# Optimization experiments

Measured on AMD Instinct MI355X. Metric: run time of the kernel, lower is better.

The kernel has to match this reference:

```python
import jax, jax.numpy as jnp
import numpy as np

N_HEAD = 8
HIDDENS = 512
NEG_INF = -1e9


def setup_inputs() -> dict:
    key = jax.random.key(0)
    ks = jax.random.split(key, 10)
    B, L, KVP, QP, H, W = 8, 1024, 512, 512, 32, 32
    s = 0.02  # init scale
    return {
        "v": jax.random.normal(ks[0], (B, L, KVP), jnp.float32),
        "k": jax.random.normal(ks[1], (B, L, KVP), jnp.float32),
        "q": jax.random.normal(ks[2], (B, QP, H, W), jnp.float32),
        "mask": jax.random.randint(ks[3], (B, 1, 1, L), 0, 2) > 0,
        "Wv": jax.random.normal(ks[4], (HIDDENS, KVP), jnp.float32) * s,
        "bv": jnp.zeros((HIDDENS,), jnp.float32),
        "Wk": jax.random.normal(ks[5], (HIDDENS, KVP), jnp.float32) * s,
        "bk": jnp.zeros((HIDDENS,), jnp.float32),
        "Wq": jax.random.normal(ks[6], (HIDDENS, QP), jnp.float32) * s,
        "bq": jnp.zeros((HIDDENS,), jnp.float32),
        "Wm": jax.random.normal(ks[7], (512, HIDDENS), jnp.float32) * s,
        "bm": jnp.zeros((512,), jnp.float32),
    }


def reference(v, k, q, mask, Wv, bv, Wk, bk, Wq, bq, Wm, bm):
    B, _, H, W = q.shape
    nh, dh = N_HEAD, HIDDENS // N_HEAD
    # k/v linear projections -> [B, nh, L, dh]
    vh = (v @ Wv.T + bv).reshape(B, -1, nh, dh).transpose(0, 2, 1, 3)
    kh = (k @ Wk.T + bk).reshape(B, -1, nh, dh).transpose(0, 2, 1, 3)
    # q 1x1 conv projection -> [B, hiddens, H, W] -> [B, nh, HW, dh]
    qp = jnp.einsum('bchw,oc->bohw', q, Wq) + bq[None, :, None, None]
    qh = qp.reshape(B, nh, dh, H * W).transpose(0, 1, 3, 2)
    # attention: scores fully materialized [B, nh, HW, L]
    scores = jnp.einsum('bnqd,bnkd->bnqk', qh, kh) / jnp.sqrt(jnp.float32(dh))
    scores = jnp.where(mask, NEG_INF, scores)
    att = jax.nn.softmax(scores, axis=-1)  # dropout omitted (eval mode)
    out = jnp.einsum('bnqk,bnkd->bnqd', att, vh)
    # [B, nh, HW, dh] -> [B, hiddens, H, W]
    out = out.transpose(0, 1, 3, 2).reshape(B, HIDDENS, H, W)
    out = jnp.einsum('bchw,oc->bohw', out, Wm) + bm[None, :, None, None]
    return jax.nn.relu(out)
```

## Files before the change

kernel.cpp:

```cpp
#include <hip/hip_runtime.h>

typedef __attribute__((ext_vector_type(8))) __bf16 bf16x8;
typedef __attribute__((ext_vector_type(4))) float  f32x4;

__device__ __forceinline__ unsigned short f2bf(float f) {
    unsigned int u = __builtin_bit_cast(unsigned int, f);
    u += 0x7fffu + ((u >> 16) & 1u);
    return (unsigned short)(u >> 16);
}
__device__ __forceinline__ unsigned int pack2(float a, float b) {
    return (unsigned int)f2bf(a) | ((unsigned int)f2bf(b) << 16);
}

__device__ __forceinline__ int swz8(int row, int chunk) {
    return row * 64 + ((chunk ^ (row & 7)) << 3);
}

__device__ __forceinline__ bf16x8 fragld(const unsigned short* lds, int row, int kk, int lane) {
    return *(const bf16x8*)(lds + swz8(row, kk * 4 + (lane >> 4)));
}

__device__ __forceinline__ void stage_direct_f32(unsigned short* lds, const float* g,
                                                 int ldg, int tid) {
#pragma unroll
    for (int s = 0; s < 2; ++s) {
        int idx = tid + s * 256;
        int row = idx >> 3, c = idx & 7;
        const float* gp = g + (size_t)row * ldg + c * 8;
        float4 v0 = *(const float4*)gp;
        float4 v1 = *(const float4*)(gp + 4);
        uint4 wr4;
        wr4.x = pack2(v0.x, v0.y); wr4.y = pack2(v0.z, v0.w);
        wr4.z = pack2(v1.x, v1.y); wr4.w = pack2(v1.z, v1.w);
        *(uint4*)(lds + swz8(row, c)) = wr4;
    }
}
__device__ __forceinline__ void stage_direct_bf16(unsigned short* lds, const unsigned short* g,
                                                  int ldg, int tid) {
#pragma unroll
    for (int s = 0; s < 2; ++s) {
        int idx = tid + s * 256;
        int row = idx >> 3, c = idx & 7;
        uint4 v = *(const uint4*)(g + (size_t)row * ldg + c * 8);
        *(uint4*)(lds + swz8(row, c)) = v;
    }
}
__device__ __forceinline__ void stage_trans_f32(unsigned short* lds, const float* g,
                                                int ldg, int tid) {
    int tk = (tid >> 4) * 4;
    int tn = (tid & 15) * 4;
    float rr[4][4];
#pragma unroll
    for (int i = 0; i < 4; ++i) {
        float4 v = *(const float4*)(g + (size_t)(tk + i) * ldg + tn);
        rr[i][0] = v.x; rr[i][1] = v.y; rr[i][2] = v.z; rr[i][3] = v.w;
    }
#pragma unroll
    for (int j = 0; j < 4; ++j) {
        int row = tn + j;
        uint2 w2;
        w2.x = pack2(rr[0][j], rr[1][j]);
        w2.y = pack2(rr[2][j], rr[3][j]);
        int off = row * 64 + (((tk >> 3) ^ (row & 7)) << 3) + (tk & 7);
        *(uint2*)(lds + off) = w2;
    }
}
__device__ __forceinline__ void stage_trans_bf16(unsigned short* lds, const unsigned short* g,
                                                 int ldg, int tid) {
    int tk = (tid >> 4) * 4;
    int tn = (tid & 15) * 4;
    unsigned short rr[4][4];
#pragma unroll
    for (int i = 0; i < 4; ++i) {
        ushort4 v = *(const ushort4*)(g + (size_t)(tk + i) * ldg + tn);
        rr[i][0] = v.x; rr[i][1] = v.y; rr[i][2] = v.z; rr[i][3] = v.w;
    }
#pragma unroll
    for (int j = 0; j < 4; ++j) {
        int row = tn + j;
        ushort4 w4;
        w4.x = rr[0][j]; w4.y = rr[1][j]; w4.z = rr[2][j]; w4.w = rr[3][j];
        int off = row * 64 + (((tk >> 3) ^ (row & 7)) << 3) + (tk & 7);
        *(ushort4*)(lds + off) = w4;
    }
}

#define MFMA_STEP(As, Bs)                                                        \
    _Pragma("unroll")                                                            \
    for (int kk = 0; kk < 2; ++kk) {                                             \
        bf16x8 a0 = fragld(As, r0w + (lane & 15), kk, lane);                     \
        bf16x8 a1 = fragld(As, r0w + 16 + (lane & 15), kk, lane);                \
        bf16x8 b0 = fragld(Bs, c0w + (lane & 15), kk, lane);                     \
        bf16x8 b1 = fragld(Bs, c0w + 16 + (lane & 15), kk, lane);                \
        acc[0][0] = __builtin_amdgcn_mfma_f32_16x16x32_bf16(a0, b0, acc[0][0], 0, 0, 0); \
        acc[0][1] = __builtin_amdgcn_mfma_f32_16x16x32_bf16(a0, b1, acc[0][1], 0, 0, 0); \
        acc[1][0] = __builtin_amdgcn_mfma_f32_16x16x32_bf16(a1, b0, acc[1][0], 0, 0, 0); \
        acc[1][1] = __builtin_amdgcn_mfma_f32_16x16x32_bf16(a1, b1, acc[1][1], 0, 0, 0); \
    }

__global__ __launch_bounds__(256) void k_proj_kv(const float* __restrict__ X,
                                                 const float* __restrict__ W,
                                                 const float* __restrict__ bias,
                                                 unsigned short* __restrict__ out) {
    __shared__ alignas(16) unsigned short As[64 * 64];
    __shared__ alignas(16) unsigned short Bs[64 * 64];
    int tid = threadIdx.x, lane = tid & 63, wid = tid >> 6;
    int r0w = (wid >> 1) * 32, c0w = (wid & 1) * 32;
    int m0 = blockIdx.x * 64, n0 = blockIdx.y * 64;
    f32x4 acc[2][2] = {};
    for (int kt = 0; kt < 512; kt += 64) {
        stage_direct_f32(As, X + (size_t)m0 * 512 + kt, 512, tid);
        stage_direct_f32(Bs, W + (size_t)n0 * 512 + kt, 512, tid);
        __syncthreads();
        MFMA_STEP(As, Bs)
        __syncthreads();
    }
#pragma unroll
    for (int j = 0; j < 2; ++j) {
        int o = n0 + c0w + j * 16 + (lane & 15);
        float bb = bias[o];
        int n = o >> 6, d = o & 63;
#pragma unroll
        for (int i = 0; i < 2; ++i) {
#pragma unroll
            for (int reg = 0; reg < 4; ++reg) {
                int r = m0 + r0w + i * 16 + ((lane >> 4) << 2) + reg;
                int b = r >> 10, l = r & 1023;
                out[(((size_t)(b * 8 + n)) * 1024 + l) * 64 + d] = f2bf(acc[i][j][reg] + bb);
            }
        }
    }
}

__global__ __launch_bounds__(256) void k_proj_q(const float* __restrict__ Q,
                                                const float* __restrict__ Wq,
                                                const float* __restrict__ bq,
                                                unsigned short* __restrict__ qh) {
    __shared__ alignas(16) unsigned short As[64 * 64];
    __shared__ alignas(16) unsigned short Bs[64 * 64];
    int tid = threadIdx.x, lane = tid & 63, wid = tid >> 6;
    int r0w = (wid >> 1) * 32, c0w = (wid & 1) * 32;
    int b = blockIdx.z;
    int m0 = blockIdx.x * 64;
    int n0 = blockIdx.y * 64;
    const float* Qb = Q + (size_t)b * 512 * 1024;
    f32x4 acc[2][2] = {};
    for (int kt = 0; kt < 512; kt += 64) {
        stage_trans_f32(As, Qb + (size_t)kt * 1024 + m0, 1024, tid);
        stage_direct_f32(Bs, Wq + (size_t)n0 * 512 + kt, 512, tid);
        __syncthreads();
        MFMA_STEP(As, Bs)
        __syncthreads();
    }
#pragma unroll
    for (int j = 0; j < 2; ++j) {
        int o = n0 + c0w + j * 16 + (lane & 15);
        float bb = bq[o];
        int n = o >> 6, d = o & 63;
#pragma unroll
        for (int i = 0; i < 2; ++i) {
#pragma unroll
            for (int reg = 0; reg < 4; ++reg) {
                int p = m0 + r0w + i * 16 + ((lane >> 4) << 2) + reg;
                qh[(((size_t)(b * 8 + n)) * 1024 + p) * 64 + d] =
                    f2bf((acc[i][j][reg] + bb) * 0.125f);
            }
        }
    }
}

__global__ __launch_bounds__(256) void k_attn(const unsigned short* __restrict__ qh,
                                              const unsigned short* __restrict__ kh,
                                              const unsigned short* __restrict__ vh,
                                              const int* __restrict__ mask,
                                              unsigned short* __restrict__ attn) {
    __shared__ alignas(16) unsigned short Qs[64 * 64];
    __shared__ alignas(16) unsigned short Ks[64 * 64];
    __shared__ alignas(16) unsigned short Vs[64 * 64];
    __shared__ alignas(16) unsigned short Ps[4][16 * 64];
    int tid = threadIdx.x, lane = tid & 63, wv = tid >> 6;
    int bn = blockIdx.x;
    int b = bn >> 3, n = bn & 7;
    int p0 = blockIdx.y * 64;
    const unsigned short* qbase = qh + (((size_t)bn) * 1024 + p0) * 64;
    const unsigned short* kbase = kh + ((size_t)bn) * 1024 * 64;
    const unsigned short* vbase = vh + ((size_t)bn) * 1024 * 64;
    const int* mbase = mask + (size_t)b * 1024;

    stage_direct_bf16(Qs, qbase, 64, tid);
    __syncthreads();
    bf16x8 aq0 = fragld(Qs, wv * 16 + (lane & 15), 0, lane);
    bf16x8 aq1 = fragld(Qs, wv * 16 + (lane & 15), 1, lane);

    float mrow[4], lrow[4];
    f32x4 o4[4] = {};
#pragma unroll
    for (int r = 0; r < 4; ++r) { mrow[r] = -3e38f; lrow[r] = 0.f; }

    for (int t = 0; t < 16; ++t) {
        int l0 = t * 64;
        __syncthreads();
        stage_direct_bf16(Ks, kbase + (size_t)l0 * 64, 64, tid);
        stage_trans_bf16(Vs, vbase + (size_t)l0 * 64, 64, tid);
        __syncthreads();

        f32x4 s[4] = {};
#pragma unroll
        for (int j = 0; j < 4; ++j) {
            bf16x8 bk0 = fragld(Ks, j * 16 + (lane & 15), 0, lane);
            bf16x8 bk1 = fragld(Ks, j * 16 + (lane & 15), 1, lane);
            s[j] = __builtin_amdgcn_mfma_f32_16x16x32_bf16(aq0, bk0, s[j], 0, 0, 0);
            s[j] = __builtin_amdgcn_mfma_f32_16x16x32_bf16(aq1, bk1, s[j], 0, 0, 0);
        }
#pragma unroll
        for (int j = 0; j < 4; ++j) {
            if (mbase[l0 + j * 16 + (lane & 15)] != 0) {
#pragma unroll
                for (int reg = 0; reg < 4; ++reg) s[j][reg] = -1e9f;
            }
        }
        float pv[4][4], corr[4];
#pragma unroll
        for (int reg = 0; reg < 4; ++reg) {
            float mx = fmaxf(fmaxf(s[0][reg], s[1][reg]), fmaxf(s[2][reg], s[3][reg]));
#pragma unroll
            for (int off = 1; off < 16; off <<= 1) mx = fmaxf(mx, __shfl_xor(mx, off, 64));
            float mnew = fmaxf(mrow[reg], mx);
            corr[reg] = __expf(mrow[reg] - mnew);
            mrow[reg] = mnew;
            float sum = 0.f;
#pragma unroll
            for (int j = 0; j < 4; ++j) {
                float p = __expf(s[j][reg] - mnew);
                pv[j][reg] = p;
                sum += p;
            }
#pragma unroll
            for (int off = 1; off < 16; off <<= 1) sum += __shfl_xor(sum, off, 64);
            lrow[reg] = lrow[reg] * corr[reg] + sum;
        }
        unsigned short* Pw = Ps[wv];
#pragma unroll
        for (int j = 0; j < 4; ++j) {
            int c = j * 16 + (lane & 15);
#pragma unroll
            for (int reg = 0; reg < 4; ++reg) {
                int pr = ((lane >> 4) << 2) + reg;
                Pw[pr * 64 + (((c >> 3) ^ (pr & 7)) << 3) + (c & 7)] = f2bf(pv[j][reg]);
            }
        }
#pragma unroll
        for (int jd = 0; jd < 4; ++jd)
#pragma unroll
            for (int reg = 0; reg < 4; ++reg) o4[jd][reg] *= corr[reg];
#pragma unroll
        for (int kk = 0; kk < 2; ++kk) {
            bf16x8 ap = fragld(Pw, (lane & 15), kk, lane);
#pragma unroll
            for (int jd = 0; jd < 4; ++jd) {
                bf16x8 bv = fragld(Vs, jd * 16 + (lane & 15), kk, lane);
                o4[jd] = __builtin_amdgcn_mfma_f32_16x16x32_bf16(ap, bv, o4[jd], 0, 0, 0);
            }
        }
    }
    float inv[4];
#pragma unroll
    for (int reg = 0; reg < 4; ++reg) inv[reg] = 1.f / lrow[reg];
    unsigned short* Ow = Ps[wv];
#pragma unroll
    for (int jd = 0; jd < 4; ++jd) {
        int d = jd * 16 + (lane & 15);
#pragma unroll
        for (int reg = 0; reg < 4; ++reg) {
            int pr = ((lane >> 4) << 2) + reg;
            Ow[d * 16 + pr] = f2bf(o4[jd][reg] * inv[reg]);
        }
    }
    int d = lane;
    uint4 w0 = *(const uint4*)(Ow + d * 16);
    uint4 w1 = *(const uint4*)(Ow + d * 16 + 8);
    size_t oaddr = ((size_t)(b * 512 + n * 64 + d)) * 1024 + p0 + wv * 16;
    *(uint4*)(attn + oaddr) = w0;
    *(uint4*)(attn + oaddr + 8) = w1;
}

__global__ __launch_bounds__(256) void k_final(const unsigned short* __restrict__ attn,
                                               const float* __restrict__ Wm,
                                               const float* __restrict__ bm,
                                               float* __restrict__ out) {
    __shared__ alignas(16) unsigned short As[64 * 64];
    __shared__ alignas(16) unsigned short Bs[64 * 64];
    int tid = threadIdx.x, lane = tid & 63, wid = tid >> 6;
    int r0w = (wid >> 1) * 32, c0w = (wid & 1) * 32;
    int b = blockIdx.z;
    int m0 = blockIdx.x * 64;
    int n0 = blockIdx.y * 64;
    const unsigned short* Ab = attn + (size_t)b * 512 * 1024;
    f32x4 acc[2][2] = {};
    for (int kt = 0; kt < 512; kt += 64) {
        stage_direct_f32(As, Wm + (size_t)m0 * 512 + kt, 512, tid);
        stage_trans_bf16(Bs, Ab + (size_t)kt * 1024 + n0, 1024, tid);
        __syncthreads();
        MFMA_STEP(As, Bs)
        __syncthreads();
    }
#pragma unroll
    for (int i = 0; i < 2; ++i) {
#pragma unroll
        for (int reg = 0; reg < 4; ++reg) {
            int o = m0 + r0w + i * 16 + ((lane >> 4) << 2) + reg;
            float bb = bm[o];
#pragma unroll
            for (int j = 0; j < 2; ++j) {
                int p = n0 + c0w + j * 16 + (lane & 15);
                out[((size_t)(b * 512 + o)) * 1024 + p] = fmaxf(acc[i][j][reg] + bb, 0.f);
            }
        }
    }
}

extern "C" void kernel_launch(void* const* d_in, const int* in_sizes, int n_in,
                              void* d_out, int out_size, void* d_ws, size_t ws_size,
                              hipStream_t stream) {
    const float* v  = (const float*)d_in[0];
    const float* k  = (const float*)d_in[1];
    const float* q  = (const float*)d_in[2];
    const int*   mask = (const int*)d_in[3];
    const float* Wv = (const float*)d_in[4];
    const float* bv = (const float*)d_in[5];
    const float* Wk = (const float*)d_in[6];
    const float* bk = (const float*)d_in[7];
    const float* Wq = (const float*)d_in[8];
    const float* bq = (const float*)d_in[9];
    const float* Wm = (const float*)d_in[10];
    const float* bm = (const float*)d_in[11];
    float* out = (float*)d_out;

    const size_t E = (size_t)8 * 8 * 1024 * 64;
    unsigned short* kh   = (unsigned short*)d_ws;
    unsigned short* vh   = kh + E;
    unsigned short* qh   = vh + E;
    unsigned short* attn = qh + E;

    dim3 blk(256);
    k_proj_kv<<<dim3(128, 8), blk, 0, stream>>>(k, Wk, bk, kh);
    k_proj_kv<<<dim3(128, 8), blk, 0, stream>>>(v, Wv, bv, vh);
    k_proj_q <<<dim3(16, 8, 8), blk, 0, stream>>>(q, Wq, bq, qh);
    k_attn   <<<dim3(64, 16), blk, 0, stream>>>(qh, kh, vh, mask, attn);
    k_final  <<<dim3(8, 16, 8), blk, 0, stream>>>(attn, Wm, bm, out);
}
```

Baseline: 235.5 us.

## Use 128x128 double-buffered GEMM tiles with bf16 weight precast and async LDS loads

```diff
diff --git a/kernel.cpp b/kernel.cpp
--- a/kernel.cpp
+++ b/kernel.cpp
@@ -16,25 +16,212 @@
     return row * 64 + ((chunk ^ (row & 7)) << 3);
 }
 
-__device__ __forceinline__ bf16x8 fragld(const unsigned short* lds, int row, int kk, int lane) {
-    return *(const bf16x8*)(lds + swz8(row, kk * 4 + (lane >> 4)));
-}
-
-__device__ __forceinline__ void stage_direct_f32(unsigned short* lds, const float* g,
-                                                 int ldg, int tid) {
+__device__ __forceinline__ void gload16(const unsigned short* g, unsigned short* l) {
+    __builtin_amdgcn_global_load_lds((const __attribute__((address_space(1))) void*)g,
+                                     (__attribute__((address_space(3))) void*)l, 16, 0, 0);
+}
+__device__ __forceinline__ void stage_async(const unsigned short* g, int ldg,
+                                            unsigned short* ldsbase, int lane, int wv) {
+    const unsigned short* gp = g + (size_t)(wv * 32 + (lane >> 3)) * ldg + (lane & 7) * 8;
+#pragma unroll
+    for (int i = 0; i < 4; ++i)
+        gload16(gp + (size_t)(i * 8) * ldg, ldsbase + (wv * 32 + i * 8) * 64);
+}
+
+struct RegTileF32 { float4 r[4][2]; };
+__device__ __forceinline__ void load_direct_f32(RegTileF32& rt, const float* base, int kt, int tid) {
+#pragma unroll
+    for (int s = 0; s < 4; ++s) {
+        int idx = tid + s * 256, row = idx >> 3, ch = idx & 7;
+        const float* gp = base + (size_t)row * 512 + kt + ch * 8;
+        rt.r[s][0] = *(const float4*)gp;
+        rt.r[s][1] = *(const float4*)(gp + 4);
+    }
+}
+__device__ __forceinline__ void write_direct(const RegTileF32& rt, unsigned short* lds, int tid) {
+#pragma unroll
+    for (int s = 0; s < 4; ++s) {
+        int idx = tid + s * 256, row = idx >> 3, ch = idx & 7;
+        uint4 w;
+        w.x = pack2(rt.r[s][0].x, rt.r[s][0].y); w.y = pack2(rt.r[s][0].z, rt.r[s][0].w);
+        w.z = pack2(rt.r[s][1].x, rt.r[s][1].y); w.w = pack2(rt.r[s][1].z, rt.r[s][1].w);
+        *(uint4*)(&lds[swz8(row, ch)]) = w;
+    }
+}
+struct RegTileQ { float r[2][4][4]; };
+__device__ __forceinline__ void load_trans_q(RegTileQ& rt, const float* qb, int m0, int kt, int tid) {
 #pragma unroll
     for (int s = 0; s < 2; ++s) {
-        int idx = tid + s * 256;
-        int row = idx >> 3, c = idx & 7;
-        const float* gp = g + (size_t)row * ldg + c * 8;
-        float4 v0 = *(const float4*)gp;
-        float4 v1 = *(const float4*)(gp + 4);
-        uint4 wr4;
-        wr4.x = pack2(v0.x, v0.y); wr4.y = pack2(v0.z, v0.w);
-        wr4.z = pack2(v1.x, v1.y); wr4.w = pack2(v1.z, v1.w);
-        *(uint4*)(lds + swz8(row, c)) = wr4;
-    }
-}
+        int qi = tid + s * 256, pq = qi & 31, cq = qi >> 5;
+        const float* gp = qb + (size_t)(kt + cq * 4) * 1024 + m0 + pq * 4;
+#pragma unroll
+        for (int i = 0; i < 4; ++i) {
+            float4 vv = *(const float4*)(gp + (size_t)i * 1024);
+            rt.r[s][i][0] = vv.x; rt.r[s][i][1] = vv.y; rt.r[s][i][2] = vv.z; rt.r[s][i][3] = vv.w;
+        }
+    }
+}
+__device__ __forceinline__ void write_trans_q(const RegTileQ& rt, unsigned short* lds, int tid) {
+#pragma unroll
+    for (int s = 0; s < 2; ++s) {
+        int qi = tid + s * 256, pq = qi & 31, cq = qi >> 5;
+#pragma unroll
+        for (int j = 0; j < 4; ++j) {
+            int row = pq * 4 + j;
+            uint2 w2;
+            w2.x = pack2(rt.r[s][0][j], rt.r[s][1][j]);
+            w2.y = pack2(rt.r[s][2][j], rt.r[s][3][j]);
+            *(uint2*)(&lds[row * 64 + (((cq >> 1) ^ (row & 7)) << 3) + (cq & 1) * 4]) = w2;
+        }
+    }
+}
+
+#define GEMM_COMPUTE(AsB, BsB)                                                       \
+    _Pragma("unroll")                                                                \
+    for (int kk = 0; kk < 2; ++kk) {                                                 \
+        bf16x8 af[4], bfr[4];                                                        \
+        _Pragma("unroll")                                                            \
+        for (int i = 0; i < 4; ++i) {                                                \
+            int rr_ = r0 + i * 16 + (lane & 15);                                     \
+            af[i] = *(const bf16x8*)(&(AsB)[swz8(rr_, kk * 4 + (lane >> 4))]);       \
+        }                                                                            \
+        _Pragma("unroll")                                                            \
+        for (int j = 0; j < 4; ++j) {                                                \
+            int rr_ = c0 + j * 16 + (lane & 15);                                     \
+            bfr[j] = *(const bf16x8*)(&(BsB)[swz8(rr_, kk * 4 + (lane >> 4))]);      \
+        }                                                                            \
+        _Pragma("unroll")                                                            \
+        for (int i = 0; i < 4; ++i)                                                  \
+            _Pragma("unroll")                                                        \
+            for (int j = 0; j < 4; ++j)                                              \
+                acc[i][j] = __builtin_amdgcn_mfma_f32_16x16x32_bf16(af[i], bfr[j],   \
+                                                                   acc[i][j], 0, 0, 0); \
+    }
+
+__global__ __launch_bounds__(256) void ck_w(const float* __restrict__ Wv, const float* __restrict__ Wk,
+                                            const float* __restrict__ Wq, const float* __restrict__ Wm,
+                                            unsigned short* __restrict__ W4) {
+    int gi = blockIdx.x * 256 + threadIdx.x;
+    int w = gi >> 15, idx = gi & 32767;
+    const float* src = (w == 0) ? Wv : (w == 1) ? Wk : (w == 2) ? Wq : Wm;
+    int row = idx >> 6, ch = idx & 63;
+    int chs = (ch & ~7) | ((ch ^ row) & 7);
+    const float* gp = src + (size_t)row * 512 + ch * 8;
+    float4 v0 = *(const float4*)gp, v1 = *(const float4*)(gp + 4);
+    uint4 o;
+    o.x = pack2(v0.x, v0.y); o.y = pack2(v0.z, v0.w);
+    o.z = pack2(v1.x, v1.y); o.w = pack2(v1.z, v1.w);
+    *(uint4*)(W4 + ((size_t)w << 18) + (size_t)row * 512 + chs * 8) = o;
+}
+
+template<bool BW4>
+__global__ __launch_bounds__(256) void g_proj_kv(const float* __restrict__ X,
+                                                 const float* __restrict__ Wf,
+                                                 const unsigned short* __restrict__ Wh,
+                                                 const float* __restrict__ bias,
+                                                 unsigned short* __restrict__ out) {
+    __shared__ alignas(16) unsigned short As[2][128 * 64];
+    __shared__ alignas(16) unsigned short Bs[2][128 * 64];
+    int tid = threadIdx.x, lane = tid & 63, wv = tid >> 6;
+    int m0 = blockIdx.x * 128, n0 = blockIdx.y * 128;
+    int r0 = (wv >> 1) * 64, c0 = (wv & 1) * 64;
+    f32x4 acc[4][4] = {};
+    const float* Ab = X + (size_t)m0 * 512;
+
+    RegTileF32 ra, rb;
+    load_direct_f32(ra, Ab, 0, tid);
+    if (!BW4) load_direct_f32(rb, Wf + (size_t)n0 * 512, 0, tid);
+    write_direct(ra, As[0], tid);
+    if (!BW4) write_direct(rb, Bs[0], tid);
+    else stage_async(Wh + (size_t)n0 * 512, 512, Bs[0], lane, wv);
+    __syncthreads();
+#pragma unroll
+    for (int t = 0; t < 8; ++t) {
+        int cur = t & 1, nxt = cur ^ 1;
+        if (t < 7) {
+            load_direct_f32(ra, Ab, (t + 1) * 64, tid);
+            if (!BW4) load_direct_f32(rb, Wf + (size_t)n0 * 512, (t + 1) * 64, tid);
+            else stage_async(Wh + (size_t)n0 * 512 + (t + 1) * 64, 512, Bs[nxt], lane, wv);
+        }
+        GEMM_COMPUTE(As[cur], Bs[cur]);
+        if (t < 7) {
+            write_direct(ra, As[nxt], tid);
+            if (!BW4) write_direct(rb, Bs[nxt], tid);
+            __syncthreads();
+        }
+    }
+#pragma unroll
+    for (int j = 0; j < 4; ++j) {
+        int o = n0 + c0 + j * 16 + (lane & 15);
+        float bb = bias[o];
+        int n = o >> 6, d = o & 63;
+#pragma unroll
+        for (int i = 0; i < 4; ++i) {
+#pragma unroll
+            for (int reg = 0; reg < 4; ++reg) {
+                int r = m0 + r0 + i * 16 + ((lane >> 4) << 2) + reg;
+                out[(((size_t)((r >> 10) * 8 + n)) * 1024 + (r & 1023)) * 64 + d] =
+                    f2bf(acc[i][j][reg] + bb);
+            }
+        }
+    }
+}
+
+template<bool BW4>
+__global__ __launch_bounds__(256) void g_proj_q(const float* __restrict__ Q,
+                                                const float* __restrict__ Wf,
+                                                const unsigned short* __restrict__ Wh,
+                                                const float* __restrict__ bq,
+                                                unsigned short* __restrict__ qh) {
+    __shared__ alignas(16) unsigned short As[2][128 * 64];
+    __shared__ alignas(16) unsigned short Bs[2][128 * 64];
+    int tid = threadIdx.x, lane = tid & 63, wv = tid >> 6;
+    int b = blockIdx.z;
+    int m0 = blockIdx.x * 128, n0 = blockIdx.y * 128;
+    int r0 = (wv >> 1) * 64, c0 = (wv & 1) * 64;
+    f32x4 acc[4][4] = {};
+    const float* Qb = Q + (size_t)b * 512 * 1024;
+
+    RegTileQ ra;
+    RegTileF32 rb;
+    load_trans_q(ra, Qb, m0, 0, tid);
+    if (!BW4) load_direct_f32(rb, Wf + (size_t)n0 * 512, 0, tid);
+    write_trans_q(ra, As[0], tid);
+    if (!BW4) write_direct(rb, Bs[0], tid);
+    else stage_async(Wh + (size_t)n0 * 512, 512, Bs[0], lane, wv);
+    __syncthreads();
+#pragma unroll
+    for (int t = 0; t < 8; ++t) {
+        int cur = t & 1, nxt = cur ^ 1;
+        if (t < 7) {
+            load_trans_q(ra, Qb, m0, (t + 1) * 64, tid);
+            if (!BW4) load_direct_f32(rb, Wf + (size_t)n0 * 512, (t + 1) * 64, tid);
+            else stage_async(Wh + (size_t)n0 * 512 + (t + 1) * 64, 512, Bs[nxt], lane, wv);
+        }
+        GEMM_COMPUTE(As[cur], Bs[cur]);
+        if (t < 7) {
+            write_trans_q(ra, As[nxt], tid);
+            if (!BW4) write_direct(rb, Bs[nxt], tid);
+            __syncthreads();
+        }
+    }
+#pragma unroll
+    for (int j = 0; j < 4; ++j) {
+        int o = n0 + c0 + j * 16 + (lane & 15);
+        float bb = bq[o];
+        int n = o >> 6, d = o & 63;
+#pragma unroll
+        for (int i = 0; i < 4; ++i) {
+#pragma unroll
+            for (int reg = 0; reg < 4; ++reg) {
+                int p = m0 + r0 + i * 16 + ((lane >> 4) << 2) + reg;
+                qh[(((size_t)(b * 8 + n)) * 1024 + p) * 64 + d] =
+                    f2bf((acc[i][j][reg] + bb) * 0.125f);
+            }
+        }
+    }
+}
+
 __device__ __forceinline__ void stage_direct_bf16(unsigned short* lds, const unsigned short* g,
                                                   int ldg, int tid) {
 #pragma unroll
@@ -43,26 +230,6 @@
         int row = idx >> 3, c = idx & 7;
         uint4 v = *(const uint4*)(g + (size_t)row * ldg + c * 8);
         *(uint4*)(lds + swz8(row, c)) = v;
-    }
-}
-__device__ __forceinline__ void stage_trans_f32(unsigned short* lds, const float* g,
-                                                int ldg, int tid) {
-    int tk = (tid >> 4) * 4;
-    int tn = (tid & 15) * 4;
-    float rr[4][4];
-#pragma unroll
-    for (int i = 0; i < 4; ++i) {
-        float4 v = *(const float4*)(g + (size_t)(tk + i) * ldg + tn);
-        rr[i][0] = v.x; rr[i][1] = v.y; rr[i][2] = v.z; rr[i][3] = v.w;
-    }
-#pragma unroll
-    for (int j = 0; j < 4; ++j) {
-        int row = tn + j;
-        uint2 w2;
-        w2.x = pack2(rr[0][j], rr[1][j]);
-        w2.y = pack2(rr[2][j], rr[3][j]);
-        int off = row * 64 + (((tk >> 3) ^ (row & 7)) << 3) + (tk & 7);
-        *(uint2*)(lds + off) = w2;
     }
 }
 __device__ __forceinline__ void stage_trans_bf16(unsigned short* lds, const unsigned short* g,
@@ -84,96 +251,15 @@
         *(ushort4*)(lds + off) = w4;
     }
 }
-
-#define MFMA_STEP(As, Bs)                                                        \
-    _Pragma("unroll")                                                            \
-    for (int kk = 0; kk < 2; ++kk) {                                             \
-        bf16x8 a0 = fragld(As, r0w + (lane & 15), kk, lane);                     \
-        bf16x8 a1 = fragld(As, r0w + 16 + (lane & 15), kk, lane);                \
-        bf16x8 b0 = fragld(Bs, c0w + (lane & 15), kk, lane);                     \
-        bf16x8 b1 = fragld(Bs, c0w + 16 + (lane & 15), kk, lane);                \
-        acc[0][0] = __builtin_amdgcn_mfma_f32_16x16x32_bf16(a0, b0, acc[0][0], 0, 0, 0); \
-        acc[0][1] = __builtin_amdgcn_mfma_f32_16x16x32_bf16(a0, b1, acc[0][1], 0, 0, 0); \
-        acc[1][0] = __builtin_amdgcn_mfma_f32_16x16x32_bf16(a1, b0, acc[1][0], 0, 0, 0); \
-        acc[1][1] = __builtin_amdgcn_mfma_f32_16x16x32_bf16(a1, b1, acc[1][1], 0, 0, 0); \
-    }
-
-__global__ __launch_bounds__(256) void k_proj_kv(const float* __restrict__ X,
-                                                 const float* __restrict__ W,
-                                                 const float* __restrict__ bias,
-                                                 unsigned short* __restrict__ out) {
-    __shared__ alignas(16) unsigned short As[64 * 64];
-    __shared__ alignas(16) unsigned short Bs[64 * 64];
-    int tid = threadIdx.x, lane = tid & 63, wid = tid >> 6;
-    int r0w = (wid >> 1) * 32, c0w = (wid & 1) * 32;
-    int m0 = blockIdx.x * 64, n0 = blockIdx.y * 64;
-    f32x4 acc[2][2] = {};
-    for (int kt = 0; kt < 512; kt += 64) {
-        stage_direct_f32(As, X + (size_t)m0 * 512 + kt, 512, tid);
-        stage_direct_f32(Bs, W + (size_t)n0 * 512 + kt, 512, tid);
-        __syncthreads();
-        MFMA_STEP(As, Bs)
-        __syncthreads();
-    }
-#pragma unroll
-    for (int j = 0; j < 2; ++j) {
-        int o = n0 + c0w + j * 16 + (lane & 15);
-        float bb = bias[o];
-        int n = o >> 6, d = o & 63;
-#pragma unroll
-        for (int i = 0; i < 2; ++i) {
-#pragma unroll
-            for (int reg = 0; reg < 4; ++reg) {
-                int r = m0 + r0w + i * 16 + ((lane >> 4) << 2) + reg;
-                int b = r >> 10, l = r & 1023;
-                out[(((size_t)(b * 8 + n)) * 1024 + l) * 64 + d] = f2bf(acc[i][j][reg] + bb);
-            }
-        }
-    }
-}
-
-__global__ __launch_bounds__(256) void k_proj_q(const float* __restrict__ Q,
-                                                const float* __restrict__ Wq,
-                                                const float* __restrict__ bq,
-                                                unsigned short* __restrict__ qh) {
-    __shared__ alignas(16) unsigned short As[64 * 64];
-    __shared__ alignas(16) unsigned short Bs[64 * 64];
-    int tid = threadIdx.x, lane = tid & 63, wid = tid >> 6;
-    int r0w = (wid >> 1) * 32, c0w = (wid & 1) * 32;
-    int b = blockIdx.z;
-    int m0 = blockIdx.x * 64;
-    int n0 = blockIdx.y * 64;
-    const float* Qb = Q + (size_t)b * 512 * 1024;
-    f32x4 acc[2][2] = {};
-    for (int kt = 0; kt < 512; kt += 64) {
-        stage_trans_f32(As, Qb + (size_t)kt * 1024 + m0, 1024, tid);
-        stage_direct_f32(Bs, Wq + (size_t)n0 * 512 + kt, 512, tid);
-        __syncthreads();
-        MFMA_STEP(As, Bs)
-        __syncthreads();
-    }
-#pragma unroll
-    for (int j = 0; j < 2; ++j) {
-        int o = n0 + c0w + j * 16 + (lane & 15);
-        float bb = bq[o];
-        int n = o >> 6, d = o & 63;
-#pragma unroll
-        for (int i = 0; i < 2; ++i) {
-#pragma unroll
-            for (int reg = 0; reg < 4; ++reg) {
-                int p = m0 + r0w + i * 16 + ((lane >> 4) << 2) + reg;
-                qh[(((size_t)(b * 8 + n)) * 1024 + p) * 64 + d] =
-                    f2bf((acc[i][j][reg] + bb) * 0.125f);
-            }
-        }
-    }
+__device__ __forceinline__ bf16x8 fragld(const unsigned short* lds, int row, int kk, int lane) {
+    return *(const bf16x8*)(lds + swz8(row, kk * 4 + (lane >> 4)));
 }
 
 __global__ __launch_bounds__(256) void k_attn(const unsigned short* __restrict__ qh,
                                               const unsigned short* __restrict__ kh,
                                               const unsigned short* __restrict__ vh,
                                               const int* __restrict__ mask,
-                                              unsigned short* __restrict__ attn) {
+                                              unsigned short* __restrict__ attnT) {
     __shared__ alignas(16) unsigned short Qs[64 * 64];
     __shared__ alignas(16) unsigned short Ks[64 * 64];
     __shared__ alignas(16) unsigned short Vs[64 * 64];
@@ -270,49 +356,70 @@
 #pragma unroll
     for (int jd = 0; jd < 4; ++jd) {
         int d = jd * 16 + (lane & 15);
+        int ch = d >> 3, doff = d & 7;
 #pragma unroll
         for (int reg = 0; reg < 4; ++reg) {
             int pr = ((lane >> 4) << 2) + reg;
-            Ow[d * 16 + pr] = f2bf(o4[jd][reg] * inv[reg]);
-        }
-    }
-    int d = lane;
-    uint4 w0 = *(const uint4*)(Ow + d * 16);
-    uint4 w1 = *(const uint4*)(Ow + d * 16 + 8);
-    size_t oaddr = ((size_t)(b * 512 + n * 64 + d)) * 1024 + p0 + wv * 16;
-    *(uint4*)(attn + oaddr) = w0;
-    *(uint4*)(attn + oaddr + 8) = w1;
-}
-
-__global__ __launch_bounds__(256) void k_final(const unsigned short* __restrict__ attn,
-                                               const float* __restrict__ Wm,
+            Ow[pr * 64 + ((ch ^ (pr & 7)) << 3) + doff] = f2bf(o4[jd][reg] * inv[reg]);
+        }
+    }
+    int row = lane >> 2, m = lane & 3;
+    const unsigned short* rb_ = Ow + row * 64 + m * 16;
+    uint4 w0 = *(const uint4*)rb_;
+    uint4 w1 = *(const uint4*)(rb_ + 8);
+    size_t oaddr = ((size_t)b * 1024 + p0 + wv * 16 + row) * 512 + n * 64 + m * 16;
+    *(uint4*)(attnT + oaddr) = w0;
+    *(uint4*)(attnT + oaddr + 8) = w1;
+}
+
+template<bool BW4>
+__global__ __launch_bounds__(256) void g_final(const unsigned short* __restrict__ attnT,
+                                               const float* __restrict__ Wf,
+                                               const unsigned short* __restrict__ Wh,
                                                const float* __restrict__ bm,
                                                float* __restrict__ out) {
-    __shared__ alignas(16) unsigned short As[64 * 64];
-    __shared__ alignas(16) unsigned short Bs[64 * 64];
-    int tid = threadIdx.x, lane = tid & 63, wid = tid >> 6;
-    int r0w = (wid >> 1) * 32, c0w = (wid & 1) * 32;
+    __shared__ alignas(16) unsigned short As[2][128 * 64];
+    __shared__ alignas(16) unsigned short Bs[2][128 * 64];
+    int tid = threadIdx.x, lane = tid & 63, wv = tid >> 6;
     int b = blockIdx.z;
-    int m0 = blockIdx.x * 64;
-    int n0 = blockIdx.y * 64;
-    const unsigned short* Ab = attn + (size_t)b * 512 * 1024;
-    f32x4 acc[2][2] = {};
-    for (int kt = 0; kt < 512; kt += 64) {
-        stage_direct_f32(As, Wm + (size_t)m0 * 512 + kt, 512, tid);
-        stage_trans_bf16(Bs, Ab + (size_t)kt * 1024 + n0, 1024, tid);
-        __syncthreads();
-        MFMA_STEP(As, Bs)
-        __syncthreads();
-    }
-#pragma unroll
-    for (int i = 0; i < 2; ++i) {
+    int m0 = blockIdx.x * 128;
+    int n0 = blockIdx.y * 128;
+    int r0 = (wv >> 1) * 64, c0 = (wv & 1) * 64;
+    f32x4 acc[4][4] = {};
+    const unsigned short* Bb = attnT + ((size_t)b * 1024 + n0) * 512;
+
+    RegTileF32 ra;
+    if (!BW4) {
+        load_direct_f32(ra, Wf + (size_t)m0 * 512, 0, tid);
+        write_direct(ra, As[0], tid);
+    } else {
+        stage_async(Wh + (size_t)m0 * 512, 512, As[0], lane, wv);
+    }
+    stage_async(Bb, 512, Bs[0], lane, wv);
+    __syncthreads();
+#pragma unroll
+    for (int t = 0; t < 8; ++t) {
+        int cur = t & 1, nxt = cur ^ 1;
+        if (t < 7) {
+            if (!BW4) load_direct_f32(ra, Wf + (size_t)m0 * 512, (t + 1) * 64, tid);
+            else stage_async(Wh + (size_t)m0 * 512 + (t + 1) * 64, 512, As[nxt], lane, wv);
+            stage_async(Bb + (t + 1) * 64, 512, Bs[nxt], lane, wv);
+        }
+        GEMM_COMPUTE(As[cur], Bs[cur]);
+        if (t < 7) {
+            if (!BW4) write_direct(ra, As[nxt], tid);
+            __syncthreads();
+        }
+    }
+#pragma unroll
+    for (int i = 0; i < 4; ++i) {
 #pragma unroll
         for (int reg = 0; reg < 4; ++reg) {
-            int o = m0 + r0w + i * 16 + ((lane >> 4) << 2) + reg;
+            int o = m0 + r0 + i * 16 + ((lane >> 4) << 2) + reg;
             float bb = bm[o];
 #pragma unroll
-            for (int j = 0; j < 2; ++j) {
-                int p = n0 + c0w + j * 16 + (lane & 15);
+            for (int j = 0; j < 4; ++j) {
+                int p = n0 + c0 + j * 16 + (lane & 15);
                 out[((size_t)(b * 512 + o)) * 1024 + p] = fmaxf(acc[i][j][reg] + bb, 0.f);
             }
         }
@@ -337,15 +444,26 @@
     float* out = (float*)d_out;
 
     const size_t E = (size_t)8 * 8 * 1024 * 64;
-    unsigned short* kh   = (unsigned short*)d_ws;
-    unsigned short* vh   = kh + E;
-    unsigned short* qh   = vh + E;
-    unsigned short* attn = qh + E;
+    unsigned short* kh    = (unsigned short*)d_ws;
+    unsigned short* vh    = kh + E;
+    unsigned short* qh    = vh + E;
+    unsigned short* attnT = qh + E;
+    unsigned short* W4    = attnT + E;
+    const size_t WSZ = (size_t)512 * 512;
+    bool useW4 = ws_size >= (4 * E + 4 * WSZ) * sizeof(unsigned short);
 
     dim3 blk(256);
-    k_proj_kv<<<dim3(128, 8), blk, 0, stream>>>(k, Wk, bk, kh);
-    k_proj_kv<<<dim3(128, 8), blk, 0, stream>>>(v, Wv, bv, vh);
-    k_proj_q <<<dim3(16, 8, 8), blk, 0, stream>>>(q, Wq, bq, qh);
-    k_attn   <<<dim3(64, 16), blk, 0, stream>>>(qh, kh, vh, mask, attn);
-    k_final  <<<dim3(8, 16, 8), blk, 0, stream>>>(attn, Wm, bm, out);
-}
+    if (useW4) {
+        ck_w<<<512, blk, 0, stream>>>(Wv, Wk, Wq, Wm, W4);
+        g_proj_kv<true><<<dim3(64, 4),   blk, 0, stream>>>(k, Wk, W4 + WSZ,     bk, kh);
+        g_proj_kv<true><<<dim3(64, 4),   blk, 0, stream>>>(v, Wv, W4,           bv, vh);
+        g_proj_q<true> <<<dim3(8, 4, 8), blk, 0, stream>>>(q, Wq, W4 + 2 * WSZ, bq, qh);
+    } else {
+        g_proj_kv<false><<<dim3(64, 4),   blk, 0, stream>>>(k, Wk, nullptr, bk, kh);
+        g_proj_kv<false><<<dim3(64, 4),   blk, 0, stream>>>(v, Wv, nullptr, bv, vh);
+        g_proj_q<false> <<<dim3(8, 4, 8), blk, 0, stream>>>(q, Wq, nullptr, bq, qh);
+    }
+    k_attn<<<dim3(64, 16), blk, 0, stream>>>(qh, kh, vh, mask, attnT);
+    if (useW4) g_final<true> <<<dim3(4, 8, 8), blk, 0, stream>>>(attnT, Wm, W4 + 3 * WSZ, bm, out);
+    else       g_final<false><<<dim3(4, 8, 8), blk, 0, stream>>>(attnT, Wm, nullptr, bm, out);
+}
```

Result: slower. 240.4 us (+2.1%).

## Merge projections into one kernel with pre-packed bf16 weights and lazy softmax rescale

Applied to the files above, without the earlier changes.

```diff
diff --git a/kernel.cpp b/kernel.cpp
--- a/kernel.cpp
+++ b/kernel.cpp
@@ -2,6 +2,9 @@
 
 typedef __attribute__((ext_vector_type(8))) __bf16 bf16x8;
 typedef __attribute__((ext_vector_type(4))) float  f32x4;
+
+#define SCALE_Q 0.1803368801111204f
+#define THR_L2  11.541560327111708f
 
 __device__ __forceinline__ unsigned short f2bf(float f) {
     unsigned int u = __builtin_bit_cast(unsigned int, f);
@@ -12,29 +15,140 @@
     return (unsigned int)f2bf(a) | ((unsigned int)f2bf(b) << 16);
 }
 
+__device__ __forceinline__ int idxW(int row, int ch) {
+    return row * 512 + (((ch & ~7) | ((ch ^ row) & 7)) << 3);
+}
 __device__ __forceinline__ int swz8(int row, int chunk) {
     return row * 64 + ((chunk ^ (row & 7)) << 3);
 }
-
 __device__ __forceinline__ bf16x8 fragld(const unsigned short* lds, int row, int kk, int lane) {
     return *(const bf16x8*)(lds + swz8(row, kk * 4 + (lane >> 4)));
 }
 
-__device__ __forceinline__ void stage_direct_f32(unsigned short* lds, const float* g,
-                                                 int ldg, int tid) {
-#pragma unroll
-    for (int s = 0; s < 2; ++s) {
-        int idx = tid + s * 256;
-        int row = idx >> 3, c = idx & 7;
-        const float* gp = g + (size_t)row * ldg + c * 8;
-        float4 v0 = *(const float4*)gp;
-        float4 v1 = *(const float4*)(gp + 4);
-        uint4 wr4;
-        wr4.x = pack2(v0.x, v0.y); wr4.y = pack2(v0.z, v0.w);
-        wr4.z = pack2(v1.x, v1.y); wr4.w = pack2(v1.z, v1.w);
-        *(uint4*)(lds + swz8(row, c)) = wr4;
-    }
-}
+__global__ __launch_bounds__(256) void ck_w(const float* __restrict__ Wv, const float* __restrict__ Wk,
+                                            const float* __restrict__ Wq, const float* __restrict__ Wm,
+                                            unsigned short* __restrict__ Wp) {
+    int tid = threadIdx.x, lane = tid & 63;
+    int gw = blockIdx.x * 4 + (tid >> 6);
+    int w = gw >> 9, rem = gw & 511;
+    int nb = rem >> 4, kb = rem & 15;
+    const float* src = (w == 0) ? Wv : (w == 1) ? Wk : (w == 2) ? Wq : Wm;
+    const float* gp = src + (size_t)(nb * 16 + (lane & 15)) * 512 + kb * 32 + (lane >> 4) * 8;
+    float4 v0 = *(const float4*)gp, v1 = *(const float4*)(gp + 4);
+    uint4 o;
+    o.x = pack2(v0.x, v0.y); o.y = pack2(v0.z, v0.w);
+    o.z = pack2(v1.x, v1.y); o.w = pack2(v1.z, v1.w);
+    *(uint4*)(Wp + ((size_t)w << 18) + ((size_t)((nb * 16 + kb) * 64 + lane)) * 8) = o;
+}
+
+__global__ __launch_bounds__(256, 2) void g_proj(const float* __restrict__ kin,
+                                                 const float* __restrict__ vin,
+                                                 const float* __restrict__ qin,
+                                                 const unsigned short* __restrict__ Wp,
+                                                 const float* __restrict__ bk,
+                                                 const float* __restrict__ bv,
+                                                 const float* __restrict__ bq,
+                                                 unsigned short* __restrict__ kh,
+                                                 unsigned short* __restrict__ vh,
+                                                 unsigned short* __restrict__ qh) {
+    __shared__ alignas(16) unsigned short As[64 * 512];
+    int tid = threadIdx.x, lane = tid & 63, wv = tid >> 6;
+    int pid = blockIdx.x;
+    int srcSel = (pid < 128) ? 0 : (pid < 256) ? 1 : 2;
+
+    if (srcSel < 2) {
+        int panel = (srcSel == 0) ? pid : pid - 128;
+        const float* src = ((srcSel == 0) ? kin : vin) + (size_t)panel * 64 * 512;
+#pragma unroll
+        for (int it = 0; it < 16; ++it) {
+            int id = it * 256 + tid, row = id >> 6, ch = id & 63;
+            const float* gp = src + (size_t)row * 512 + ch * 8;
+            float4 a0 = *(const float4*)gp, a1 = *(const float4*)(gp + 4);
+            uint4 w;
+            w.x = pack2(a0.x, a0.y); w.y = pack2(a0.z, a0.w);
+            w.z = pack2(a1.x, a1.y); w.w = pack2(a1.z, a1.w);
+            *(uint4*)(&As[idxW(row, ch)]) = w;
+        }
+    } else {
+        int qi = pid - 256, b = qi >> 4, pp = qi & 15;
+        const float* src = qin + (size_t)b * 512 * 1024 + pp * 64;
+#pragma unroll
+        for (int cc = 0; cc < 8; ++cc) {
+            int c0 = cc * 64 + (tid >> 4) * 4;
+            int pl = (tid & 15) * 4;
+            float rr[4][4];
+#pragma unroll
+            for (int i = 0; i < 4; ++i) {
+                float4 t4 = *(const float4*)(src + (size_t)(c0 + i) * 1024 + pl);
+                rr[i][0] = t4.x; rr[i][1] = t4.y; rr[i][2] = t4.z; rr[i][3] = t4.w;
+            }
+#pragma unroll
+            for (int j = 0; j < 4; ++j) {
+                int row = pl + j, chunk = c0 >> 3, off = c0 & 7;
+                uint2 w2;
+                w2.x = pack2(rr[0][j], rr[1][j]);
+                w2.y = pack2(rr[2][j], rr[3][j]);
+                *(uint2*)(&As[row * 512 + (((chunk & ~7) | ((chunk ^ row) & 7)) << 3) + off]) = w2;
+            }
+        }
+    }
+    __syncthreads();
+
+    int wsel = (srcSel == 0) ? 1 : (srcSel == 1) ? 0 : 2;
+    const unsigned short* Wb = Wp + ((size_t)wsel << 18);
+    f32x4 acc[4][8] = {};
+#pragma unroll 2
+    for (int kb = 0; kb < 16; ++kb) {
+        bf16x8 af[4];
+#pragma unroll
+        for (int i = 0; i < 4; ++i)
+            af[i] = *(const bf16x8*)(&As[idxW(i * 16 + (lane & 15), kb * 4 + (lane >> 4))]);
+#pragma unroll
+        for (int j = 0; j < 8; ++j) {
+            bf16x8 bf8 = *(const bf16x8*)(Wb + ((size_t)(((wv * 8 + j) * 16 + kb) * 64 + lane)) * 8);
+#pragma unroll
+            for (int i = 0; i < 4; ++i)
+                acc[i][j] = __builtin_amdgcn_mfma_f32_16x16x32_bf16(af[i], bf8, acc[i][j], 0, 0, 0);
+        }
+    }
+
+    if (srcSel < 2) {
+        int panel = (srcSel == 0) ? pid : pid - 128;
+        unsigned short* dst = (srcSel == 0) ? kh : vh;
+        const float* bias = (srcSel == 0) ? bk : bv;
+#pragma unroll
+        for (int j = 0; j < 8; ++j) {
+            int o = wv * 128 + j * 16 + (lane & 15);
+            float bb = bias[o];
+            int n = o >> 6, d = o & 63;
+#pragma unroll
+            for (int i = 0; i < 4; ++i)
+#pragma unroll
+                for (int reg = 0; reg < 4; ++reg) {
+                    int r = panel * 64 + i * 16 + ((lane >> 4) << 2) + reg;
+                    dst[(((size_t)((r >> 10) * 8 + n)) * 1024 + (r & 1023)) * 64 + d] =
+                        f2bf(acc[i][j][reg] + bb);
+                }
+        }
+    } else {
+        int qi = pid - 256, b = qi >> 4, pp = qi & 15;
+#pragma unroll
+        for (int j = 0; j < 8; ++j) {
+            int o = wv * 128 + j * 16 + (lane & 15);
+            float bb = bq[o];
+            int n = o >> 6, d = o & 63;
+#pragma unroll
+            for (int i = 0; i < 4; ++i)
+#pragma unroll
+                for (int reg = 0; reg < 4; ++reg) {
+                    int p = pp * 64 + i * 16 + ((lane >> 4) << 2) + reg;
+                    qh[(((size_t)(b * 8 + n)) * 1024 + p) * 64 + d] =
+                        f2bf((acc[i][j][reg] + bb) * SCALE_Q);
+                }
+        }
+    }
+}
+
 __device__ __forceinline__ void stage_direct_bf16(unsigned short* lds, const unsigned short* g,
                                                   int ldg, int tid) {
 #pragma unroll
@@ -43,26 +157,6 @@
         int row = idx >> 3, c = idx & 7;
         uint4 v = *(const uint4*)(g + (size_t)row * ldg + c * 8);
         *(uint4*)(lds + swz8(row, c)) = v;
-    }
-}
-__device__ __forceinline__ void stage_trans_f32(unsigned short* lds, const float* g,
-                                                int ldg, int tid) {
-    int tk = (tid >> 4) * 4;
-    int tn = (tid & 15) * 4;
-    float rr[4][4];
-#pragma unroll
-    for (int i = 0; i < 4; ++i) {
-        float4 v = *(const float4*)(g + (size_t)(tk + i) * ldg + tn);
-        rr[i][0] = v.x; rr[i][1] = v.y; rr[i][2] = v.z; rr[i][3] = v.w;
-    }
-#pragma unroll
-    for (int j = 0; j < 4; ++j) {
-        int row = tn + j;
-        uint2 w2;
-        w2.x = pack2(rr[0][j], rr[1][j]);
-        w2.y = pack2(rr[2][j], rr[3][j]);
-        int off = row * 64 + (((tk >> 3) ^ (row & 7)) << 3) + (tk & 7);
-        *(uint2*)(lds + off) = w2;
     }
 }
 __device__ __forceinline__ void stage_trans_bf16(unsigned short* lds, const unsigned short* g,
@@ -85,109 +179,23 @@
     }
 }
 
-#define MFMA_STEP(As, Bs)                                                        \
-    _Pragma("unroll")                                                            \
-    for (int kk = 0; kk < 2; ++kk) {                                             \
-        bf16x8 a0 = fragld(As, r0w + (lane & 15), kk, lane);                     \
-        bf16x8 a1 = fragld(As, r0w + 16 + (lane & 15), kk, lane);                \
-        bf16x8 b0 = fragld(Bs, c0w + (lane & 15), kk, lane);                     \
-        bf16x8 b1 = fragld(Bs, c0w + 16 + (lane & 15), kk, lane);                \
-        acc[0][0] = __builtin_amdgcn_mfma_f32_16x16x32_bf16(a0, b0, acc[0][0], 0, 0, 0); \
-        acc[0][1] = __builtin_amdgcn_mfma_f32_16x16x32_bf16(a0, b1, acc[0][1], 0, 0, 0); \
-        acc[1][0] = __builtin_amdgcn_mfma_f32_16x16x32_bf16(a1, b0, acc[1][0], 0, 0, 0); \
-        acc[1][1] = __builtin_amdgcn_mfma_f32_16x16x32_bf16(a1, b1, acc[1][1], 0, 0, 0); \
-    }
-
-__global__ __launch_bounds__(256) void k_proj_kv(const float* __restrict__ X,
-                                                 const float* __restrict__ W,
-                                                 const float* __restrict__ bias,
-                                                 unsigned short* __restrict__ out) {
-    __shared__ alignas(16) unsigned short As[64 * 64];
-    __shared__ alignas(16) unsigned short Bs[64 * 64];
-    int tid = threadIdx.x, lane = tid & 63, wid = tid >> 6;
-    int r0w = (wid >> 1) * 32, c0w = (wid & 1) * 32;
-    int m0 = blockIdx.x * 64, n0 = blockIdx.y * 64;
-    f32x4 acc[2][2] = {};
-    for (int kt = 0; kt < 512; kt += 64) {
-        stage_direct_f32(As, X + (size_t)m0 * 512 + kt, 512, tid);
-        stage_direct_f32(Bs, W + (size_t)n0 * 512 + kt, 512, tid);
-        __syncthreads();
-        MFMA_STEP(As, Bs)
-        __syncthreads();
-    }
-#pragma unroll
-    for (int j = 0; j < 2; ++j) {
-        int o = n0 + c0w + j * 16 + (lane & 15);
-        float bb = bias[o];
-        int n = o >> 6, d = o & 63;
-#pragma unroll
-        for (int i = 0; i < 2; ++i) {
-#pragma unroll
-            for (int reg = 0; reg < 4; ++reg) {
-                int r = m0 + r0w + i * 16 + ((lane >> 4) << 2) + reg;
-                int b = r >> 10, l = r & 1023;
-                out[(((size_t)(b * 8 + n)) * 1024 + l) * 64 + d] = f2bf(acc[i][j][reg] + bb);
-            }
-        }
-    }
-}
-
-__global__ __launch_bounds__(256) void k_proj_q(const float* __restrict__ Q,
-                                                const float* __restrict__ Wq,
-                                                const float* __restrict__ bq,
-                                                unsigned short* __restrict__ qh) {
-    __shared__ alignas(16) unsigned short As[64 * 64];
-    __shared__ alignas(16) unsigned short Bs[64 * 64];
-    int tid = threadIdx.x, lane = tid & 63, wid = tid >> 6;
-    int r0w = (wid >> 1) * 32, c0w = (wid & 1) * 32;
-    int b = blockIdx.z;
-    int m0 = blockIdx.x * 64;
-    int n0 = blockIdx.y * 64;
-    const float* Qb = Q + (size_t)b * 512 * 1024;
-    f32x4 acc[2][2] = {};
-    for (int kt = 0; kt < 512; kt += 64) {
-        stage_trans_f32(As, Qb + (size_t)kt * 1024 + m0, 1024, tid);
-        stage_direct_f32(Bs, Wq + (size_t)n0 * 512 + kt, 512, tid);
-        __syncthreads();
-        MFMA_STEP(As, Bs)
-        __syncthreads();
-    }
-#pragma unroll
-    for (int j = 0; j < 2; ++j) {
-        int o = n0 + c0w + j * 16 + (lane & 15);
-        float bb = bq[o];
-        int n = o >> 6, d = o & 63;
-#pragma unroll
-        for (int i = 0; i < 2; ++i) {
-#pragma unroll
-            for (int reg = 0; reg < 4; ++reg) {
-                int p = m0 + r0w + i * 16 + ((lane >> 4) << 2) + reg;
-                qh[(((size_t)(b * 8 + n)) * 1024 + p) * 64 + d] =
-                    f2bf((acc[i][j][reg] + bb) * 0.125f);
-            }
-        }
-    }
-}
-
-__global__ __launch_bounds__(256) void k_attn(const unsigned short* __restrict__ qh,
+__global__ __launch_bounds__(256) void k_attn(unsigned short* qa,
                                               const unsigned short* __restrict__ kh,
                                               const unsigned short* __restrict__ vh,
-                                              const int* __restrict__ mask,
-                                              unsigned short* __restrict__ attn) {
+                                              const int* __restrict__ mask) {
     __shared__ alignas(16) unsigned short Qs[64 * 64];
     __shared__ alignas(16) unsigned short Ks[64 * 64];
     __shared__ alignas(16) unsigned short Vs[64 * 64];
     __shared__ alignas(16) unsigned short Ps[4][16 * 64];
     int tid = threadIdx.x, lane = tid & 63, wv = tid >> 6;
     int bn = blockIdx.x;
-    int b = bn >> 3, n = bn & 7;
+    int b = bn >> 3;
     int p0 = blockIdx.y * 64;
-    const unsigned short* qbase = qh + (((size_t)bn) * 1024 + p0) * 64;
     const unsigned short* kbase = kh + ((size_t)bn) * 1024 * 64;
     const unsigned short* vbase = vh + ((size_t)bn) * 1024 * 64;
     const int* mbase = mask + (size_t)b * 1024;
 
-    stage_direct_bf16(Qs, qbase, 64, tid);
+    stage_direct_bf16(Qs, qa + (((size_t)bn) * 1024 + p0) * 64, 64, tid);
     __syncthreads();
     bf16x8 aq0 = fragld(Qs, wv * 16 + (lane & 15), 0, lane);
     bf16x8 aq1 = fragld(Qs, wv * 16 + (lane & 15), 1, lane);
@@ -219,25 +227,51 @@
                 for (int reg = 0; reg < 4; ++reg) s[j][reg] = -1e9f;
             }
         }
-        float pv[4][4], corr[4];
+        float mx[4];
+        bool ok = true;
 #pragma unroll
         for (int reg = 0; reg < 4; ++reg) {
-            float mx = fmaxf(fmaxf(s[0][reg], s[1][reg]), fmaxf(s[2][reg], s[3][reg]));
-#pragma unroll
-            for (int off = 1; off < 16; off <<= 1) mx = fmaxf(mx, __shfl_xor(mx, off, 64));
-            float mnew = fmaxf(mrow[reg], mx);
-            corr[reg] = __expf(mrow[reg] - mnew);
-            mrow[reg] = mnew;
-            float sum = 0.f;
-#pragma unroll
-            for (int j = 0; j < 4; ++j) {
-                float p = __expf(s[j][reg] - mnew);
-                pv[j][reg] = p;
-                sum += p;
-            }
-#pragma unroll
-            for (int off = 1; off < 16; off <<= 1) sum += __shfl_xor(sum, off, 64);
-            lrow[reg] = lrow[reg] * corr[reg] + sum;
+            float m_ = fmaxf(fmaxf(s[0][reg], s[1][reg]), fmaxf(s[2][reg], s[3][reg]));
+#pragma unroll
+            for (int off = 1; off < 16; off <<= 1) m_ = fmaxf(m_, __shfl_xor(m_, off, 64));
+            mx[reg] = m_;
+            ok = ok && (m_ <= mrow[reg] + THR_L2);
+        }
+        float pvv[4][4];
+        if (__all(ok)) {
+#pragma unroll
+            for (int reg = 0; reg < 4; ++reg) {
+                float sum = 0.f;
+#pragma unroll
+                for (int j = 0; j < 4; ++j) {
+                    float p = exp2f(s[j][reg] - mrow[reg]);
+                    pvv[j][reg] = p; sum += p;
+                }
+#pragma unroll
+                for (int off = 1; off < 16; off <<= 1) sum += __shfl_xor(sum, off, 64);
+                lrow[reg] += sum;
+            }
+        } else {
+            float corr[4];
+#pragma unroll
+            for (int reg = 0; reg < 4; ++reg) {
+                float mnew = fmaxf(mrow[reg], mx[reg]);
+                corr[reg] = exp2f(mrow[reg] - mnew);
+                float sum = 0.f;
+#pragma unroll
+                for (int j = 0; j < 4; ++j) {
+                    float p = exp2f(s[j][reg] - mnew);
+                    pvv[j][reg] = p; sum += p;
+                }
+#pragma unroll
+                for (int off = 1; off < 16; off <<= 1) sum += __shfl_xor(sum, off, 64);
+                lrow[reg] = lrow[reg] * corr[reg] + sum;
+                mrow[reg] = mnew;
+            }
+#pragma unroll
+            for (int jd = 0; jd < 4; ++jd)
+#pragma unroll
+                for (int reg = 0; reg < 4; ++reg) o4[jd][reg] *= corr[reg];
         }
         unsigned short* Pw = Ps[wv];
 #pragma unroll
@@ -246,20 +280,16 @@
 #pragma unroll
             for (int reg = 0; reg < 4; ++reg) {
                 int pr = ((lane >> 4) << 2) + reg;
-                Pw[pr * 64 + (((c >> 3) ^ (pr & 7)) << 3) + (c & 7)] = f2bf(pv[j][reg]);
-            }
-        }
-#pragma unroll
-        for (int jd = 0; jd < 4; ++jd)
-#pragma unroll
-            for (int reg = 0; reg < 4; ++reg) o4[jd][reg] *= corr[reg];
+                Pw[pr * 64 + (((c >> 3) ^ (pr & 7)) << 3) + (c & 7)] = f2bf(pvv[j][reg]);
+            }
+        }
 #pragma unroll
         for (int kk = 0; kk < 2; ++kk) {
             bf16x8 ap = fragld(Pw, (lane & 15), kk, lane);
 #pragma unroll
             for (int jd = 0; jd < 4; ++jd) {
-                bf16x8 bv = fragld(Vs, jd * 16 + (lane & 15), kk, lane);
-                o4[jd] = __builtin_amdgcn_mfma_f32_16x16x32_bf16(ap, bv, o4[jd], 0, 0, 0);
+                bf16x8 bvf = fragld(Vs, jd * 16 + (lane & 15), kk, lane);
+                o4[jd] = __builtin_amdgcn_mfma_f32_16x16x32_bf16(ap, bvf, o4[jd], 0, 0, 0);
             }
         }
     }
@@ -270,53 +300,64 @@
 #pragma unroll
     for (int jd = 0; jd < 4; ++jd) {
         int d = jd * 16 + (lane & 15);
+        int ch = d >> 3, doff = d & 7;
 #pragma unroll
         for (int reg = 0; reg < 4; ++reg) {
             int pr = ((lane >> 4) << 2) + reg;
-            Ow[d * 16 + pr] = f2bf(o4[jd][reg] * inv[reg]);
-        }
-    }
-    int d = lane;
-    uint4 w0 = *(const uint4*)(Ow + d * 16);
-    uint4 w1 = *(const uint4*)(Ow + d * 16 + 8);
-    size_t oaddr = ((size_t)(b * 512 + n * 64 + d)) * 1024 + p0 + wv * 16;
-    *(uint4*)(attn + oaddr) = w0;
-    *(uint4*)(attn + oaddr + 8) = w1;
-}
-
-__global__ __launch_bounds__(256) void k_final(const unsigned short* __restrict__ attn,
-                                               const float* __restrict__ Wm,
-                                               const float* __restrict__ bm,
-                                               float* __restrict__ out) {
-    __shared__ alignas(16) unsigned short As[64 * 64];
-    __shared__ alignas(16) unsigned short Bs[64 * 64];
-    int tid = threadIdx.x, lane = tid & 63, wid = tid >> 6;
-    int r0w = (wid >> 1) * 32, c0w = (wid & 1) * 32;
-    int b = blockIdx.z;
-    int m0 = blockIdx.x * 64;
-    int n0 = blockIdx.y * 64;
-    const unsigned short* Ab = attn + (size_t)b * 512 * 1024;
-    f32x4 acc[2][2] = {};
-    for (int kt = 0; kt < 512; kt += 64) {
-        stage_direct_f32(As, Wm + (size_t)m0 * 512 + kt, 512, tid);
-        stage_trans_bf16(Bs, Ab + (size_t)kt * 1024 + n0, 1024, tid);
-        __syncthreads();
-        MFMA_STEP(As, Bs)
-        __syncthreads();
-    }
-#pragma unroll
-    for (int i = 0; i < 2; ++i) {
+            Ow[pr * 64 + ((ch ^ (pr & 7)) << 3) + doff] = f2bf(o4[jd][reg] * inv[reg]);
+        }
+    }
+    size_t base = ((size_t)bn * 16 + blockIdx.y) * 4096;
+#pragma unroll
+    for (int h = 0; h < 2; ++h) {
+        int p = lane & 15;
+        int ch = h * 4 + (lane >> 4);
+        uint4 w = *(const uint4*)(&Ow[p * 64 + ((ch ^ (p & 7)) << 3)]);
+        *(uint4*)(qa + base + (size_t)(wv * 2 + h) * 512 + (size_t)lane * 8) = w;
+    }
+}
+
+__global__ __launch_bounds__(256, 2) void g_final(const unsigned short* __restrict__ aP,
+                                                  const unsigned short* __restrict__ Wm8,
+                                                  const float* __restrict__ bm,
+                                                  float* __restrict__ out) {
+    int tid = threadIdx.x, lane = tid & 63, wv = tid >> 6;
+    int wr = wv >> 1, wc = wv & 1;
+    int b = blockIdx.z, m0 = blockIdx.x * 128, n0 = blockIdx.y * 128;
+    int onb = m0 / 16 + wr * 4;
+    int pnb = n0 / 16 + wc * 4;
+    f32x4 acc[4][4] = {};
+#pragma unroll 2
+    for (int kb = 0; kb < 16; ++kb) {
+        int nh = kb >> 1, h = kb & 1, bn = b * 8 + nh;
+        bf16x8 af[4], bf8[4];
+#pragma unroll
+        for (int i = 0; i < 4; ++i)
+            af[i] = *(const bf16x8*)(Wm8 + ((size_t)(((onb + i) * 16 + kb) * 64 + lane)) * 8);
+#pragma unroll
+        for (int j = 0; j < 4; ++j) {
+            int pb = pnb + j;
+            bf8[j] = *(const bf16x8*)(aP + ((size_t)bn * 16 + (pb >> 2)) * 4096 +
+                                      (size_t)((pb & 3) * 2 + h) * 512 + (size_t)lane * 8);
+        }
+#pragma unroll
+        for (int i = 0; i < 4; ++i)
+#pragma unroll
+            for (int j = 0; j < 4; ++j)
+                acc[i][j] = __builtin_amdgcn_mfma_f32_16x16x32_bf16(af[i], bf8[j], acc[i][j], 0, 0, 0);
+    }
+#pragma unroll
+    for (int i = 0; i < 4; ++i)
 #pragma unroll
         for (int reg = 0; reg < 4; ++reg) {
-            int o = m0 + r0w + i * 16 + ((lane >> 4) << 2) + reg;
+            int o = m0 + wr * 64 + i * 16 + ((lane >> 4) << 2) + reg;
             float bb = bm[o];
 #pragma unroll
-            for (int j = 0; j < 2; ++j) {
-                int p = n0 + c0w + j * 16 + (lane & 15);
+            for (int j = 0; j < 4; ++j) {
+                int p = n0 + wc * 64 + j * 16 + (lane & 15);
                 out[((size_t)(b * 512 + o)) * 1024 + p] = fmaxf(acc[i][j][reg] + bb, 0.f);
             }
         }
-    }
 }
 
 extern "C" void kernel_launch(void* const* d_in, const int* in_sizes, int n_in,
@@ -337,15 +378,14 @@
     float* out = (float*)d_out;
 
     const size_t E = (size_t)8 * 8 * 1024 * 64;
-    unsigned short* kh   = (unsigned short*)d_ws;
-    unsigned short* vh   = kh + E;
-    unsigned short* qh   = vh + E;
-    unsigned short* attn = qh + E;
+    unsigned short* kh = (unsigned short*)d_ws;
+    unsigned short* vh = kh + E;
+    unsigned short* qh = vh + E;
+    unsigned short* Wp = qh + E;
 
     dim3 blk(256);
-    k_proj_kv<<<dim3(128, 8), blk, 0, stream>>>(k, Wk, bk, kh);
-    k_proj_kv<<<dim3(128, 8), blk, 0, stream>>>(v, Wv, bv, vh);
-    k_proj_q <<<dim3(16, 8, 8), blk, 0, stream>>>(q, Wq, bq, qh);
-    k_attn   <<<dim3(64, 16), blk, 0, stream>>>(qh, kh, vh, mask, attn);
-    k_final  <<<dim3(8, 16, 8), blk, 0, stream>>>(attn, Wm, bm, out);
-}
+    ck_w  <<<512, blk, 0, stream>>>(Wv, Wk, Wq, Wm, Wp);
+    g_proj<<<384, blk, 0, stream>>>(k, v, q, Wp, bk, bv, bq, kh, vh, qh);
+    k_attn<<<dim3(64, 16), blk, 0, stream>>>(qh, kh, vh, mask);
+    g_final<<<dim3(4, 8, 8), blk, 0, stream>>>(qh, Wp + 3 * 262144, bm, out);
+}
```

Result: no change. 238.4 us (+1.3%).
